# Kernel optimization log

Measured on AMD Instinct MI355X. Metric: run time of the kernel, lower is better.

The kernel has to match this reference:

```python
import jax, jax.numpy as jnp
import numpy as np

B, N, D, H = 32, 8192, 128, 128


def setup_inputs() -> dict:
    key = jax.random.key(0)
    ks = jax.random.split(key, 9)
    s = lambda k, shp, fan: jax.random.normal(k, shp, jnp.float32) / np.sqrt(fan)
    return {
        "x": jax.random.normal(ks[0], (B, N, D), jnp.float32),
        "Wg1": s(ks[1], (D, H), D), "bg1": jnp.zeros((H,), jnp.float32),
        "Wg2": s(ks[2], (H, 1), H), "bg2": jnp.zeros((1,), jnp.float32),
        "Wn1": s(ks[3], (D, H), D), "bn1": jnp.zeros((H,), jnp.float32),
        "Wn2": s(ks[4], (H, H), H), "bn2": jnp.zeros((H,), jnp.float32),
    }


def reference(x, Wg1, bg1, Wg2, bg2, Wn1, bn1, Wn2, bn2):
    # gate_nn: Linear -> SiLU -> Linear(->1); scores per node
    gate = jnp.einsum("bnd,dh->bnh", x, Wg1) + bg1
    gate = jax.nn.silu(gate)
    gate = jnp.einsum("bnh,ho->bno", gate, Wg2) + bg2  # [B,N,1]
    # nn: Linear -> SiLU -> Linear; transformed node features
    h = jax.nn.silu(jnp.einsum("bnd,dh->bnh", x, Wn1) + bn1)
    h = jnp.einsum("bnh,hk->bnk", h, Wn2) + bn2  # [B,N,H]
    # segment softmax over nodes of each graph (segments == batch dim here)
    attn = jax.nn.softmax(gate, axis=1)  # [B,N,1]
    # weighted-sum pooling per graph
    return jnp.sum(attn * h, axis=1)  # [B,H]
```

## Files before the change

### kernel.cpp

```cpp
#include <hip/hip_runtime.h>

#define B_ 32
#define N_ 8192
#define D_ 128
#define H_ 128
#define R_ (B_ * N_)

#define TILES 8
#define NBLK 512

typedef _Float16 f16;
typedef __attribute__((ext_vector_type(4))) _Float16 f16x4;
typedef __attribute__((ext_vector_type(8))) _Float16 f16x8;
typedef __attribute__((ext_vector_type(4))) float f32x4;

static constexpr size_t WPACK_OFF = 0;
static constexpr size_t VPART_OFF = 65536;
static constexpr size_t SPART_OFF = VPART_OFF + (size_t)NBLK * 128 * 4;

__device__ __forceinline__ float silu_f(float v) {
    return v * __builtin_amdgcn_rcpf(1.0f + __expf(-v));
}

__device__ __forceinline__ f32x4 mfma16(f16x8 a, f16x8 b, f32x4 c) {
    return __builtin_amdgcn_mfma_f32_16x16x32_f16(a, b, c, 0, 0, 0);
}

__global__ void k0_prepack(const float* __restrict__ Wg1,
                           const float* __restrict__ Wn1,
                           f16* __restrict__ wp) {
    int tid = blockIdx.x * 256 + threadIdx.x;
    int m    = tid >> 14;
    int r    = tid & 16383;
    int j    = r & 7;
    int lane = (r >> 3) & 63;
    int kc   = (r >> 9) & 3;
    int nt   = r >> 11;
    int k = kc * 32 + (lane >> 4) * 8 + j;
    int n = nt * 16 + (lane & 15);
    const float* W = m ? Wn1 : Wg1;
    wp[tid] = (f16)W[k * 128 + n];
}

__global__ __launch_bounds__(512, 4) void k1_fused(
        const float* __restrict__ x,
        const float* __restrict__ bg1, const float* __restrict__ wg2,
        const float* __restrict__ bg2, const float* __restrict__ bn1,
        const f16* __restrict__ wp,
        float* __restrict__ vpart, float* __restrict__ spart) {
    __shared__ f16 xlds[64 * 128];
    __shared__ float gpart[8][64];

    const int tid  = threadIdx.x;
    const int w    = tid >> 6;
    const int lane = tid & 63;
    const int q    = lane >> 4;
    const int c    = lane & 15;

    const float4* xg = (const float4*)x + (long)blockIdx.x * (64 * TILES) * 32;

    float4 xv[4];
#pragma unroll
    for (int s = 0; s < 4; ++s) xv[s] = xg[s * 512 + tid];

    const f16x8* wpv = (const f16x8*)wp;
    f16x8 fg1[4], fn1[4];
#pragma unroll
    for (int kc = 0; kc < 4; ++kc) {
        int base = (w * 4 + kc) * 64 + lane;
        fg1[kc] = wpv[base];
        fn1[kc] = wpv[2048 + base];
    }
    float bg1q[4], wg2q[4], bn1q[4];
#pragma unroll
    for (int r = 0; r < 4; ++r) {
        int col = w * 16 + q * 4 + r;
        bg1q[r] = bg1[col];
        wg2q[r] = wg2[col];
        bn1q[r] = bn1[col];
    }
    const float bg2v = bg2[0];

    const int loh_e = (q * 16 + (c ^ q)) * 8;
    const int loh_o = (q * 16 + (c ^ (q | 4))) * 8;

#pragma unroll
    for (int s = 0; s < 4; ++s) {
        int e   = s * 512 + tid;
        int row = e >> 5, c4 = e & 31;
        int mt = row >> 4, cc = row & 15;
        int kc = c4 >> 3, qq = (c4 >> 1) & 3, j = (c4 & 1) * 4;
        int sw = (c4 >> 1) & 7;
        float4 vv = xv[s];
        f16x4 hv = {(f16)vv.x, (f16)vv.y, (f16)vv.z, (f16)vv.w};
        *(f16x4*)&xlds[((mt * 4 + kc) * 64 + qq * 16 + (cc ^ sw)) * 8 + j] = hv;
    }
    if (TILES > 1) {
#pragma unroll
        for (int s = 0; s < 4; ++s) xv[s] = xg[2048 + s * 512 + tid];
    }

    float V[4] = {0.f, 0.f, 0.f, 0.f};
    float Sacc = 0.f;

    __syncthreads();

#pragma unroll 1
    for (int t = 0; t < TILES; ++t) {
        f16x4 hq[4];
#pragma unroll
        for (int mt = 0; mt < 4; ++mt) {
            f16x8 a[4];
#pragma unroll
            for (int kc = 0; kc < 4; ++kc)
                a[kc] = *(const f16x8*)&xlds[(mt * 4 + kc) * 512 +
                                             ((kc & 1) ? loh_o : loh_e)];
            f32x4 ag = {0.f, 0.f, 0.f, 0.f};
            f32x4 an = {0.f, 0.f, 0.f, 0.f};
#pragma unroll
            for (int kc = 0; kc < 4; ++kc) {
                ag = mfma16(fg1[kc], a[kc], ag);
                an = mfma16(fn1[kc], a[kc], an);
            }
            f16x4 h4;
#pragma unroll
            for (int r = 0; r < 4; ++r) h4[r] = (f16)silu_f(an[r] + bn1q[r]);
            hq[mt] = h4;
            float p = 0.f;
#pragma unroll
            for (int r = 0; r < 4; ++r)
                p += silu_f(ag[r] + bg1q[r]) * wg2q[r];
            p += __shfl_xor(p, 16);
            p += __shfl_xor(p, 32);
            if (lane < 16) gpart[w][mt * 16 + lane] = p;
        }
        __syncthreads();

#pragma unroll
        for (int mt = 0; mt < 4; ++mt) {
            float g = bg2v;
#pragma unroll
            for (int k = 0; k < 8; ++k) g += gpart[k][mt * 16 + c];
            float e4 = __expf(g);
            Sacc += e4;
#pragma unroll
            for (int r = 0; r < 4; ++r)
                V[r] += e4 * (float)hq[mt][r];
        }

        if (t + 1 < TILES) {
#pragma unroll
            for (int s = 0; s < 4; ++s) {
                int e   = s * 512 + tid;
                int row = e >> 5, c4 = e & 31;
                int mt = row >> 4, cc = row & 15;
                int kc = c4 >> 3, qq = (c4 >> 1) & 3, j = (c4 & 1) * 4;
                int sw = (c4 >> 1) & 7;
                float4 vv = xv[s];
                f16x4 hv = {(f16)vv.x, (f16)vv.y, (f16)vv.z, (f16)vv.w};
                *(f16x4*)&xlds[((mt * 4 + kc) * 64 + qq * 16 + (cc ^ sw)) * 8 + j] = hv;
            }
            if (t + 2 < TILES) {
#pragma unroll
                for (int s = 0; s < 4; ++s)
                    xv[s] = xg[(t + 2) * 2048 + s * 512 + tid];
            }
            __syncthreads();
        }
    }

#pragma unroll
    for (int m = 1; m < 16; m <<= 1)
#pragma unroll
        for (int r = 0; r < 4; ++r) V[r] += __shfl_xor(V[r], m);
    if (c == 0) {
        float4 o = {V[0], V[1], V[2], V[3]};
        *(float4*)&vpart[(long)blockIdx.x * 128 + w * 16 + q * 4] = o;
    }
    if (w == 0) {
        float Sl = Sacc;
#pragma unroll
        for (int m = 1; m < 16; m <<= 1) Sl += __shfl_xor(Sl, m);
        if (lane == 0) spart[blockIdx.x] = Sl;
    }
}

__global__ void k2_combine(const float* __restrict__ vpart,
                           const float* __restrict__ spart,
                           const float* __restrict__ Wn2,
                           const float* __restrict__ bn2,
                           float* __restrict__ out) {
    const int b = blockIdx.x;
    const int t = threadIdx.x;

    __shared__ float pooled[128];
    __shared__ float sred;

    float v = 0.f;
    if (t < 128) {
        const float* vp = vpart + (long)b * 16 * 128;
#pragma unroll
        for (int k = 0; k < 16; ++k) v += vp[k * 128 + t];
    }

    float s = (t < 16) ? spart[b * 16 + t] : 0.f;
#pragma unroll
    for (int m = 1; m < 16; m <<= 1) s += __shfl_xor(s, m);
    if (t == 0) sred = s;
    __syncthreads();

    if (t < 128) pooled[t] = v / sred;
    __syncthreads();
    if (t < 128) {
        float acc = bn2[t];
#pragma unroll 8
        for (int k = 0; k < 128; ++k) acc += pooled[k] * Wn2[k * 128 + t];
        out[b * 128 + t] = acc;
    }
}

extern "C" void kernel_launch(void* const* d_in, const int* in_sizes, int n_in,
                              void* d_out, int out_size, void* d_ws, size_t ws_size,
                              hipStream_t stream) {
    const float* x   = (const float*)d_in[0];
    const float* Wg1 = (const float*)d_in[1];
    const float* bg1 = (const float*)d_in[2];
    const float* Wg2 = (const float*)d_in[3];
    const float* bg2 = (const float*)d_in[4];
    const float* Wn1 = (const float*)d_in[5];
    const float* bn1 = (const float*)d_in[6];
    const float* Wn2 = (const float*)d_in[7];
    const float* bn2 = (const float*)d_in[8];
    float* out = (float*)d_out;

    char* ws = (char*)d_ws;
    f16*   wp    = (f16*)(ws + WPACK_OFF);
    float* vpart = (float*)(ws + VPART_OFF);
    float* spart = (float*)(ws + SPART_OFF);

    k0_prepack<<<128, 256, 0, stream>>>(Wg1, Wn1, wp);
    k1_fused<<<NBLK, 512, 0, stream>>>(x, bg1, Wg2, bg2, bn1, wp, vpart, spart);
    k2_combine<<<32, 256, 0, stream>>>(vpart, spart, Wn2, bn2, out);
}
```

Before: 235.9 us.

## Stream x tiles into double-buffered LDS via async global-to-LDS loads

Drops register staging and the fp32-to-fp16 repack of x tiles into LDS. The kernel now issues direct global_load_lds 16-byte transfers into two fp32 LDS buffers with an XOR swizzle, prefetching tile t+1 while tile t is computed. The fp16 conversion moves to the MFMA operand read path. Syncs become raw barriers with explicit waitcnts. The cost is twice the LDS footprint (about 66KB per block) and double the LDS read bytes, plus conversion work inside the inner loop.

```diff
diff --git a/kernel.cpp b/kernel.cpp
--- a/kernel.cpp
+++ b/kernel.cpp
@@ -25,6 +25,17 @@
 __device__ __forceinline__ f32x4 mfma16(f16x8 a, f16x8 b, f32x4 c) {
     return __builtin_amdgcn_mfma_f32_16x16x32_f16(a, b, c, 0, 0, 0);
 }
+
+__device__ __forceinline__ void gload_lds16(const float* g, float* l) {
+    __builtin_amdgcn_global_load_lds(
+        (const __attribute__((address_space(1))) void*)g,
+        (__attribute__((address_space(3))) void*)l, 16, 0, 0);
+}
+
+#define ASM_VMCNT0() asm volatile("s_waitcnt vmcnt(0)" ::: "memory")
+#define ASM_LGKM0()  asm volatile("s_waitcnt lgkmcnt(0)" ::: "memory")
+#define RAW_BAR()    __builtin_amdgcn_s_barrier()
+#define SCHED0()     __builtin_amdgcn_sched_barrier(0)
 
 __global__ void k0_prepack(const float* __restrict__ Wg1,
                            const float* __restrict__ Wn1,
@@ -48,7 +59,7 @@
         const float* __restrict__ bg2, const float* __restrict__ bn1,
         const f16* __restrict__ wp,
         float* __restrict__ vpart, float* __restrict__ spart) {
-    __shared__ f16 xlds[64 * 128];
+    __shared__ float xbuf[2][64 * 128];
     __shared__ float gpart[8][64];
 
     const int tid  = threadIdx.x;
@@ -57,11 +68,19 @@
     const int q    = lane >> 4;
     const int c    = lane & 15;
 
-    const float4* xg = (const float4*)x + (long)blockIdx.x * (64 * TILES) * 32;
-
-    float4 xv[4];
-#pragma unroll
-    for (int s = 0; s < 4; ++s) xv[s] = xg[s * 512 + tid];
+    const float* xblk = x + (long)blockIdx.x * (64 * TILES) * 128;
+
+    int off[4], dst[4];
+#pragma unroll
+    for (int i = 0; i < 4; ++i) {
+        int row = w * 8 + i * 2 + (lane >> 5);
+        int seg = (lane & 31) ^ (row & 7);
+        off[i] = row * 128 + seg * 4;
+        dst[i] = (w * 4 + i) * 256;
+    }
+
+#pragma unroll
+    for (int i = 0; i < 4; ++i) gload_lds16(xblk + off[i], &xbuf[0][dst[i]]);
 
     const f16x8* wpv = (const f16x8*)wp;
     f16x8 fg1[4], fn1[4];
@@ -80,41 +99,40 @@
         bn1q[r] = bn1[col];
     }
     const float bg2v = bg2[0];
-
-    const int loh_e = (q * 16 + (c ^ q)) * 8;
-    const int loh_o = (q * 16 + (c ^ (q | 4))) * 8;
-
-#pragma unroll
-    for (int s = 0; s < 4; ++s) {
-        int e   = s * 512 + tid;
-        int row = e >> 5, c4 = e & 31;
-        int mt = row >> 4, cc = row & 15;
-        int kc = c4 >> 3, qq = (c4 >> 1) & 3, j = (c4 & 1) * 4;
-        int sw = (c4 >> 1) & 7;
-        float4 vv = xv[s];
-        f16x4 hv = {(f16)vv.x, (f16)vv.y, (f16)vv.z, (f16)vv.w};
-        *(f16x4*)&xlds[((mt * 4 + kc) * 64 + qq * 16 + (cc ^ sw)) * 8 + j] = hv;
-    }
-    if (TILES > 1) {
-#pragma unroll
-        for (int s = 0; s < 4; ++s) xv[s] = xg[2048 + s * 512 + tid];
-    }
+    const int vr = c & 7;
 
     float V[4] = {0.f, 0.f, 0.f, 0.f};
     float Sacc = 0.f;
 
-    __syncthreads();
+    ASM_VMCNT0();
+    RAW_BAR();
+    SCHED0();
 
 #pragma unroll 1
     for (int t = 0; t < TILES; ++t) {
+        const int cur = t & 1;
+        if (t + 1 < TILES) {
+            const float* xt = xblk + (t + 1) * (64 * 128);
+            float* bufN = &xbuf[cur ^ 1][0];
+#pragma unroll
+            for (int i = 0; i < 4; ++i) gload_lds16(xt + off[i], bufN + dst[i]);
+        }
+
+        const float4* bp = (const float4*)&xbuf[cur][0];
         f16x4 hq[4];
 #pragma unroll
         for (int mt = 0; mt < 4; ++mt) {
+            const int r32 = (mt * 16 + c) * 32;
             f16x8 a[4];
 #pragma unroll
-            for (int kc = 0; kc < 4; ++kc)
-                a[kc] = *(const f16x8*)&xlds[(mt * 4 + kc) * 512 +
-                                             ((kc & 1) ? loh_o : loh_e)];
+            for (int kc = 0; kc < 4; ++kc) {
+                int s0 = kc * 8 + q * 2;
+                float4 f0 = bp[r32 + (s0 ^ vr)];
+                float4 f1 = bp[r32 + ((s0 + 1) ^ vr)];
+                f16x8 av = {(f16)f0.x, (f16)f0.y, (f16)f0.z, (f16)f0.w,
+                            (f16)f1.x, (f16)f1.y, (f16)f1.z, (f16)f1.w};
+                a[kc] = av;
+            }
             f32x4 ag = {0.f, 0.f, 0.f, 0.f};
             f32x4 an = {0.f, 0.f, 0.f, 0.f};
 #pragma unroll
@@ -134,7 +152,9 @@
             p += __shfl_xor(p, 32);
             if (lane < 16) gpart[w][mt * 16 + lane] = p;
         }
-        __syncthreads();
+        ASM_LGKM0();
+        RAW_BAR();
+        SCHED0();
 
 #pragma unroll
         for (int mt = 0; mt < 4; ++mt) {
@@ -147,26 +167,10 @@
             for (int r = 0; r < 4; ++r)
                 V[r] += e4 * (float)hq[mt][r];
         }
-
-        if (t + 1 < TILES) {
-#pragma unroll
-            for (int s = 0; s < 4; ++s) {
-                int e   = s * 512 + tid;
-                int row = e >> 5, c4 = e & 31;
-                int mt = row >> 4, cc = row & 15;
-                int kc = c4 >> 3, qq = (c4 >> 1) & 3, j = (c4 & 1) * 4;
-                int sw = (c4 >> 1) & 7;
-                float4 vv = xv[s];
-                f16x4 hv = {(f16)vv.x, (f16)vv.y, (f16)vv.z, (f16)vv.w};
-                *(f16x4*)&xlds[((mt * 4 + kc) * 64 + qq * 16 + (cc ^ sw)) * 8 + j] = hv;
-            }
-            if (t + 2 < TILES) {
-#pragma unroll
-                for (int s = 0; s < 4; ++s)
-                    xv[s] = xg[(t + 2) * 2048 + s * 512 + tid];
-            }
-            __syncthreads();
-        }
+        ASM_LGKM0();
+        ASM_VMCNT0();
+        RAW_BAR();
+        SCHED0();
     }
 
 #pragma unroll
```

Measured after the change: 225.4 us. 4.4% less time.
